# Kernel optimization log

Hardware: AMD Instinct MI355X
Metric: run time of the kernel (lower is better)

Reference implementation:

```python
import jax, jax.numpy as jnp
import numpy as np

N_NODES = 2048
N_EDGES = 32768
N_IN = 256
MSG_HID = 512
MSG_OUT = 256
N_HID = 512


def _linear_params(key, fan_in, fan_out):
    kw, kb = jax.random.split(key)
    bound = 1.0 / np.sqrt(fan_in)
    W = jax.random.uniform(kw, (fan_out, fan_in), jnp.float32, -bound, bound)
    b = jax.random.uniform(kb, (fan_out,), jnp.float32, -bound, bound)
    return W, b


def setup_inputs() -> dict:
    key = jax.random.key(0)
    ks = jax.random.split(key, 8)
    inputs = jax.random.normal(ks[0], (N_NODES, N_IN), jnp.float32)
    # one-hot incidence matrices built from random receiver/sender node indices
    recv_idx = jax.random.randint(ks[1], (N_EDGES,), 0, N_NODES)
    send_idx = jax.random.randint(ks[2], (N_EDGES,), 0, N_NODES)
    rel_rec = jax.nn.one_hot(recv_idx, N_NODES, dtype=jnp.float32)   # [E, N]
    rel_send = jax.nn.one_hot(send_idx, N_NODES, dtype=jnp.float32)  # [E, N]
    msg_W1, msg_b1 = _linear_params(ks[3], 2 * N_IN, MSG_HID)
    msg_W2, msg_b2 = _linear_params(ks[4], MSG_HID, MSG_OUT)
    out_W1, out_b1 = _linear_params(ks[5], N_IN + MSG_OUT, N_HID)
    out_W2, out_b2 = _linear_params(ks[6], N_HID, N_HID)
    out_W3, out_b3 = _linear_params(ks[7], N_HID, N_IN)
    return {
        'inputs': inputs, 'rel_rec': rel_rec, 'rel_send': rel_send,
        'msg_W1': msg_W1, 'msg_b1': msg_b1, 'msg_W2': msg_W2, 'msg_b2': msg_b2,
        'out_W1': out_W1, 'out_b1': out_b1, 'out_W2': out_W2, 'out_b2': out_b2,
        'out_W3': out_W3, 'out_b3': out_b3,
    }


def reference(inputs, rel_rec, rel_send, msg_W1, msg_b1, msg_W2, msg_b2,
              out_W1, out_b1, out_W2, out_b2, out_W3, out_b3):
    # gather node features to edges via dense one-hot matmuls (as in original)
    receivers = rel_rec @ inputs    # [E, n_in]
    senders = rel_send @ inputs     # [E, n_in]
    pre_msg = jnp.concatenate([senders, receivers], axis=1)  # [E, 2*n_in]
    # edge-message MLP (dropout p=0 -> identity)
    msg = jax.nn.relu(pre_msg @ msg_W1.T + msg_b1)
    msg = jax.nn.relu(msg @ msg_W2.T + msg_b2)               # [E, msg_out]
    # scatter-add messages to receiving nodes: (msg^T @ rel_rec)^T == rel_rec^T @ msg
    agg_msgs = rel_rec.T @ msg                               # [N, msg_out]
    aug_inputs = jnp.concatenate([inputs, agg_msgs], axis=-1)
    # node-update MLP
    pred = jax.nn.relu(aug_inputs @ out_W1.T + out_b1)
    pred = jax.nn.relu(pred @ out_W2.T + out_b2)
    pred = pred @ out_W3.T + out_b3
    return inputs + pred
```

## Files before the change

### kernel.cpp

```cpp
#include <hip/hip_runtime.h>
#include <hip/hip_bf16.h>
#include <stdint.h>

using bf16 = __hip_bfloat16;
typedef short bf16x8 __attribute__((ext_vector_type(8)));
typedef float floatx4 __attribute__((ext_vector_type(4)));

static constexpr int NODES = 2048;
static constexpr int EDGES = 32768;

__device__ inline uint4 cvt8(const float* __restrict__ p) {
    const float4* f = (const float4*)p;
    float4 a = f[0], b = f[1];
    union { uint4 u; bf16 h[8]; } pk;
    pk.h[0] = __float2bfloat16(a.x); pk.h[1] = __float2bfloat16(a.y);
    pk.h[2] = __float2bfloat16(a.z); pk.h[3] = __float2bfloat16(a.w);
    pk.h[4] = __float2bfloat16(b.x); pk.h[5] = __float2bfloat16(b.y);
    pk.h[6] = __float2bfloat16(b.z); pk.h[7] = __float2bfloat16(b.w);
    return pk.u;
}

template<int BM, int BN, int AMODE, int BMODE, int EPI>
__device__ __forceinline__ void gemm_body(
    const bf16* __restrict__ A, const float* __restrict__ Af,
    const float* __restrict__ Bt, const float* __restrict__ bias,
    bf16* __restrict__ Cout, float* __restrict__ OutF,
    const float* __restrict__ inputsF, const float* __restrict__ UV,
    const float* __restrict__ b1v, const int* __restrict__ sidx,
    const int* __restrict__ ridx, const float* __restrict__ aggin,
    float* __restrict__ aggout, int M, int N, int K, int bx, int by)
{
    constexpr int BK = 32;
    constexpr int PA = BM / 64;
    constexpr int PB = BN / 64;
    constexpr int MI = BM / 32;
    constexpr int NJ = BN / 32;
    __shared__ bf16 As[BM * BK];
    __shared__ bf16 Bs[BN * BK];
    __shared__ int sIdx[BM];
    __shared__ int rIdx[BM];

    const int t = threadIdx.x;
    const int m0 = by * BM;
    const int n0 = bx * BN;

    if constexpr (AMODE == 3) {
        if (t < BM) {
            sIdx[t] = sidx[m0 + t] & (NODES - 1);
            rIdx[t] = ridx[m0 + t] & (NODES - 1);
        }
        __syncthreads();
    }

    const int sr = t >> 2;
    const int sc = t & 3;

    uint4 ra[PA], rb[PB];

    auto loadTiles = [&](int kt) {
        const int kk = kt * BK + sc * 8;
#pragma unroll
        for (int p = 0; p < PA; ++p) {
            const int row = p * 64 + sr;
            if constexpr (AMODE == 0) {
                ra[p] = *(const uint4*)(A + (size_t)(m0 + row) * K + kk);
            } else if constexpr (AMODE == 1) {
                ra[p] = cvt8(Af + (size_t)(m0 + row) * K + kk);
            } else if constexpr (AMODE == 2) {
                const float* src = (kk < 256)
                    ? (inputsF + (size_t)(m0 + row) * 256 + kk)
                    : (aggin + (size_t)(m0 + row) * 256 + (kk - 256));
                ra[p] = cvt8(src);
            } else {
                const float4* u = (const float4*)(UV + (size_t)sIdx[row] * 1024 + kk);
                const float4* v = (const float4*)(UV + (size_t)rIdx[row] * 1024 + 512 + kk);
                const float4* c = (const float4*)(b1v + kk);
                float4 u0 = u[0], u1 = u[1], v0 = v[0], v1 = v[1], c0 = c[0], c1 = c[1];
                union { uint4 q; bf16 h[8]; } pk;
                pk.h[0] = __float2bfloat16(fmaxf(u0.x + v0.x + c0.x, 0.f));
                pk.h[1] = __float2bfloat16(fmaxf(u0.y + v0.y + c0.y, 0.f));
                pk.h[2] = __float2bfloat16(fmaxf(u0.z + v0.z + c0.z, 0.f));
                pk.h[3] = __float2bfloat16(fmaxf(u0.w + v0.w + c0.w, 0.f));
                pk.h[4] = __float2bfloat16(fmaxf(u1.x + v1.x + c1.x, 0.f));
                pk.h[5] = __float2bfloat16(fmaxf(u1.y + v1.y + c1.y, 0.f));
                pk.h[6] = __float2bfloat16(fmaxf(u1.z + v1.z + c1.z, 0.f));
                pk.h[7] = __float2bfloat16(fmaxf(u1.w + v1.w + c1.w, 0.f));
                ra[p] = pk.q;
            }
        }
#pragma unroll
        for (int p = 0; p < PB; ++p) {
            const int row = p * 64 + sr;
            if constexpr (BMODE == 0) {
                rb[p] = cvt8(Bt + (size_t)(n0 + row) * K + kk);
            } else {
                const int n = n0 + row;
                rb[p] = cvt8(Bt + (size_t)(n & 511) * 512 + (n >> 9) * 256 + kk);
            }
        }
    };

    const int wv = t >> 6;
    const int lane = t & 63;
    const int wm = wv >> 1, wn = wv & 1;
    const int r16 = lane & 15, q = lane >> 4;

    floatx4 acc[MI][NJ] = {};

    loadTiles(0);
    const int KT = K / BK;
    for (int kt = 0; kt < KT; ++kt) {
        __syncthreads();
#pragma unroll
        for (int p = 0; p < PA; ++p)
            *(uint4*)(&As[(p * 64 + sr) * BK + sc * 8]) = ra[p];
#pragma unroll
        for (int p = 0; p < PB; ++p)
            *(uint4*)(&Bs[(p * 64 + sr) * BK + sc * 8]) = rb[p];
        __syncthreads();
        if (kt + 1 < KT) loadTiles(kt + 1);

        bf16x8 af[MI], bfr[NJ];
#pragma unroll
        for (int i = 0; i < MI; ++i)
            af[i] = *(const bf16x8*)(&As[(wm * (BM / 2) + i * 16 + r16) * BK + q * 8]);
#pragma unroll
        for (int j = 0; j < NJ; ++j)
            bfr[j] = *(const bf16x8*)(&Bs[(wn * (BN / 2) + j * 16 + r16) * BK + q * 8]);
#pragma unroll
        for (int i = 0; i < MI; ++i)
#pragma unroll
            for (int j = 0; j < NJ; ++j)
                acc[i][j] = __builtin_amdgcn_mfma_f32_16x16x32_bf16(af[i], bfr[j], acc[i][j], 0, 0, 0);
    }

    float bv[NJ];
#pragma unroll
    for (int j = 0; j < NJ; ++j)
        bv[j] = (EPI == 3) ? 0.f : bias[n0 + wn * (BN / 2) + j * 16 + r16];

#pragma unroll
    for (int i = 0; i < MI; ++i) {
        const int lr = wm * (BM / 2) + i * 16 + q * 4;
        const int rbase = m0 + lr;
#pragma unroll
        for (int j = 0; j < NJ; ++j) {
            const int gc = n0 + wn * (BN / 2) + j * 16 + r16;
#pragma unroll
            for (int r = 0; r < 4; ++r) {
                float v = acc[i][j][r] + bv[j];
                const int gr = rbase + r;
                if constexpr (EPI == 0) {
                    v = fmaxf(v, 0.0f);
                    Cout[(size_t)gr * N + gc] = __float2bfloat16(v);
                } else if constexpr (EPI == 1) {
                    v = fmaxf(v, 0.0f);
                    atomicAdd(&aggout[(size_t)rIdx[lr + r] * 256 + gc], v);
                } else if constexpr (EPI == 2) {
                    OutF[(size_t)gr * 256 + gc] = inputsF[(size_t)gr * 256 + gc] + v;
                } else {
                    OutF[(size_t)gr * N + gc] = v;
                }
            }
        }
    }
}

template<int BM, int BN, int AMODE, int BMODE, int EPI>
__global__ __launch_bounds__(256, 2) void gemm_k(
    const bf16* __restrict__ A, const float* __restrict__ Af,
    const float* __restrict__ Bt, const float* __restrict__ bias,
    bf16* __restrict__ Cout, float* __restrict__ OutF,
    const float* __restrict__ inputsF, const float* __restrict__ UV,
    const float* __restrict__ b1v, const int* __restrict__ sidx,
    const int* __restrict__ ridx, const float* __restrict__ aggin,
    float* __restrict__ aggout, int M, int N, int K)
{
    gemm_body<BM, BN, AMODE, BMODE, EPI>(A, Af, Bt, bias, Cout, OutF, inputsF,
        UV, b1v, sidx, ridx, aggin, aggout, M, N, K, blockIdx.x, blockIdx.y);
}

__global__ __launch_bounds__(256) void fat_pre(
    const float* __restrict__ rel_rec, const float* __restrict__ rel_send,
    int* __restrict__ recv_idx, int* __restrict__ send_idx,
    float4* __restrict__ agg, const float* __restrict__ inputs,
    const float* __restrict__ msg_W1, float* __restrict__ UV)
{
    const int b = blockIdx.x;
    if (b < 16384) {
        const int half = b >> 13;
        const int rb = b & 8191;
        const float* mat = half ? rel_send : rel_rec;
        int* out = half ? send_idx : recv_idx;
        const int w = threadIdx.x >> 6;
        const int lane = threadIdx.x & 63;
        const int row = rb * 4 + w;
        if (lane == 0) out[row] = 0;
        const uint4* base = (const uint4*)(mat + (size_t)row * NODES);
        for (int p = 0; p < 8; ++p) {
            uint4 v = base[p * 64 + lane];
            const bool hit = (v.x | v.y | v.z | v.w) != 0u;
            if (hit) {
                int e = v.x ? 0 : (v.y ? 1 : (v.z ? 2 : 3));
                out[row] = p * 256 + lane * 4 + e;
            }
            if (__any(hit)) break;
        }
    } else if (b < 16896) {
        agg[(size_t)(b - 16384) * 256 + threadIdx.x] = float4{0.f, 0.f, 0.f, 0.f};
    } else {
        const int g = b - 16896;
        gemm_body<64, 64, 1, 1, 3>(nullptr, inputs, msg_W1, nullptr, nullptr, UV,
            nullptr, nullptr, nullptr, nullptr, nullptr, nullptr, nullptr,
            NODES, 1024, 256, g & 15, g >> 4);
    }
}

extern "C" void kernel_launch(void* const* d_in, const int* in_sizes, int n_in,
                              void* d_out, int out_size, void* d_ws, size_t ws_size,
                              hipStream_t stream) {
    const float* inputs   = (const float*)d_in[0];
    const float* rel_rec  = (const float*)d_in[1];
    const float* rel_send = (const float*)d_in[2];
    const float* msg_W1   = (const float*)d_in[3];
    const float* msg_b1   = (const float*)d_in[4];
    const float* msg_W2   = (const float*)d_in[5];
    const float* msg_b2   = (const float*)d_in[6];
    const float* out_W1   = (const float*)d_in[7];
    const float* out_b1   = (const float*)d_in[8];
    const float* out_W2   = (const float*)d_in[9];
    const float* out_b2   = (const float*)d_in[10];
    const float* out_W3   = (const float*)d_in[11];
    const float* out_b3   = (const float*)d_in[12];

    char* ws = (char*)d_ws;
    int*   recv_idx = (int*)(ws + 0);
    int*   send_idx = (int*)(ws + 131072);
    float* agg      = (float*)(ws + 262144);
    float* UV       = (float*)(ws + 2359296);
    bf16*  g1       = (bf16*)(ws + 10747904);
    bf16*  g2       = (bf16*)(ws + 12845056);
    if (ws_size < (size_t)16 * 1024 * 1024) return;

    fat_pre<<<17408, 256, 0, stream>>>(rel_rec, rel_send, recv_idx, send_idx,
                                       (float4*)agg, inputs, msg_W1, UV);

    gemm_k<128, 128, 3, 0, 1><<<dim3(2, 256), 256, 0, stream>>>(
        nullptr, nullptr, msg_W2, msg_b2, nullptr, nullptr,
        nullptr, UV, msg_b1, send_idx, recv_idx, nullptr, agg,
        EDGES, 256, 512);

    gemm_k<64, 64, 2, 0, 0><<<dim3(8, 32), 256, 0, stream>>>(
        nullptr, nullptr, out_W1, out_b1, g1, nullptr,
        inputs, nullptr, nullptr, nullptr, nullptr, agg, nullptr,
        NODES, 512, 512);

    gemm_k<64, 64, 0, 0, 0><<<dim3(8, 32), 256, 0, stream>>>(
        g1, nullptr, out_W2, out_b2, g2, nullptr,
        nullptr, nullptr, nullptr, nullptr, nullptr, nullptr, nullptr,
        NODES, 512, 512);

    gemm_k<64, 64, 0, 0, 2><<<dim3(4, 32), 256, 0, stream>>>(
        g2, nullptr, out_W3, out_b3, nullptr, (float*)d_out,
        inputs, nullptr, nullptr, nullptr, nullptr, nullptr, nullptr,
        NODES, 256, 512);
}
```

Before: 602.6 us.

## Store per-node UV projections in bf16 and retile edge GEMM to 64x256

The per-node first-layer projections (UV) are now written in bf16 instead of fp32, which halves the bytes of the random-row gathers the edge-message GEMM does per edge. The gathered values are widened back to fp32 by bit-shifting before the bias add and ReLU. The edge GEMM also changes from 128x128 tiles on a 2x256 grid to 64x256 tiles on a 1x512 grid, so each gathered row is loaded once across all 256 output columns instead of twice. The cost is extra rounding of UV to bf16 before the add, which costs some accuracy, and a larger accumulator tile per wave.

```diff
diff --git a/kernel.cpp b/kernel.cpp
--- a/kernel.cpp
+++ b/kernel.cpp
@@ -25,7 +25,7 @@
     const bf16* __restrict__ A, const float* __restrict__ Af,
     const float* __restrict__ Bt, const float* __restrict__ bias,
     bf16* __restrict__ Cout, float* __restrict__ OutF,
-    const float* __restrict__ inputsF, const float* __restrict__ UV,
+    const float* __restrict__ inputsF, const bf16* __restrict__ UVb,
     const float* __restrict__ b1v, const int* __restrict__ sidx,
     const int* __restrict__ ridx, const float* __restrict__ aggin,
     float* __restrict__ aggout, int M, int N, int K, int bx, int by)
@@ -72,19 +72,20 @@
                     : (aggin + (size_t)(m0 + row) * 256 + (kk - 256));
                 ra[p] = cvt8(src);
             } else {
-                const float4* u = (const float4*)(UV + (size_t)sIdx[row] * 1024 + kk);
-                const float4* v = (const float4*)(UV + (size_t)rIdx[row] * 1024 + 512 + kk);
+                union { uint4 q; unsigned short h[8]; } uu, vv;
+                uu.q = *(const uint4*)(UVb + (size_t)sIdx[row] * 1024 + kk);
+                vv.q = *(const uint4*)(UVb + (size_t)rIdx[row] * 1024 + 512 + kk);
                 const float4* c = (const float4*)(b1v + kk);
-                float4 u0 = u[0], u1 = u[1], v0 = v[0], v1 = v[1], c0 = c[0], c1 = c[1];
+                float4 c0 = c[0], c1 = c[1];
+                const float cf[8] = {c0.x, c0.y, c0.z, c0.w, c1.x, c1.y, c1.z, c1.w};
                 union { uint4 q; bf16 h[8]; } pk;
-                pk.h[0] = __float2bfloat16(fmaxf(u0.x + v0.x + c0.x, 0.f));
-                pk.h[1] = __float2bfloat16(fmaxf(u0.y + v0.y + c0.y, 0.f));
-                pk.h[2] = __float2bfloat16(fmaxf(u0.z + v0.z + c0.z, 0.f));
-                pk.h[3] = __float2bfloat16(fmaxf(u0.w + v0.w + c0.w, 0.f));
-                pk.h[4] = __float2bfloat16(fmaxf(u1.x + v1.x + c1.x, 0.f));
-                pk.h[5] = __float2bfloat16(fmaxf(u1.y + v1.y + c1.y, 0.f));
-                pk.h[6] = __float2bfloat16(fmaxf(u1.z + v1.z + c1.z, 0.f));
-                pk.h[7] = __float2bfloat16(fmaxf(u1.w + v1.w + c1.w, 0.f));
+#pragma unroll
+                for (int e = 0; e < 8; ++e) {
+                    union { unsigned int u; float f; } a2, b2;
+                    a2.u = (unsigned int)uu.h[e] << 16;
+                    b2.u = (unsigned int)vv.h[e] << 16;
+                    pk.h[e] = __float2bfloat16(fmaxf(a2.f + b2.f + cf[e], 0.f));
+                }
                 ra[p] = pk.q;
             }
         }
@@ -137,7 +138,7 @@
     float bv[NJ];
 #pragma unroll
     for (int j = 0; j < NJ; ++j)
-        bv[j] = (EPI == 3) ? 0.f : bias[n0 + wn * (BN / 2) + j * 16 + r16];
+        bv[j] = (EPI == 3 || EPI == 4) ? 0.f : bias[n0 + wn * (BN / 2) + j * 16 + r16];
 
 #pragma unroll
     for (int i = 0; i < MI; ++i) {
@@ -158,8 +159,10 @@
                     atomicAdd(&aggout[(size_t)rIdx[lr + r] * 256 + gc], v);
                 } else if constexpr (EPI == 2) {
                     OutF[(size_t)gr * 256 + gc] = inputsF[(size_t)gr * 256 + gc] + v;
+                } else if constexpr (EPI == 3) {
+                    OutF[(size_t)gr * N + gc] = v;
                 } else {
-                    OutF[(size_t)gr * N + gc] = v;
+                    Cout[(size_t)gr * N + gc] = __float2bfloat16(v);
                 }
             }
         }
@@ -171,20 +174,20 @@
     const bf16* __restrict__ A, const float* __restrict__ Af,
     const float* __restrict__ Bt, const float* __restrict__ bias,
     bf16* __restrict__ Cout, float* __restrict__ OutF,
-    const float* __restrict__ inputsF, const float* __restrict__ UV,
+    const float* __restrict__ inputsF, const bf16* __restrict__ UVb,
     const float* __restrict__ b1v, const int* __restrict__ sidx,
     const int* __restrict__ ridx, const float* __restrict__ aggin,
     float* __restrict__ aggout, int M, int N, int K)
 {
     gemm_body<BM, BN, AMODE, BMODE, EPI>(A, Af, Bt, bias, Cout, OutF, inputsF,
-        UV, b1v, sidx, ridx, aggin, aggout, M, N, K, blockIdx.x, blockIdx.y);
+        UVb, b1v, sidx, ridx, aggin, aggout, M, N, K, blockIdx.x, blockIdx.y);
 }
 
 __global__ __launch_bounds__(256) void fat_pre(
     const float* __restrict__ rel_rec, const float* __restrict__ rel_send,
     int* __restrict__ recv_idx, int* __restrict__ send_idx,
     float4* __restrict__ agg, const float* __restrict__ inputs,
-    const float* __restrict__ msg_W1, float* __restrict__ UV)
+    const float* __restrict__ msg_W1, bf16* __restrict__ UVb)
 {
     const int b = blockIdx.x;
     if (b < 16384) {
@@ -210,7 +213,7 @@
         agg[(size_t)(b - 16384) * 256 + threadIdx.x] = float4{0.f, 0.f, 0.f, 0.f};
     } else {
         const int g = b - 16896;
-        gemm_body<64, 64, 1, 1, 3>(nullptr, inputs, msg_W1, nullptr, nullptr, UV,
+        gemm_body<64, 64, 1, 1, 4>(nullptr, inputs, msg_W1, nullptr, UVb, nullptr,
             nullptr, nullptr, nullptr, nullptr, nullptr, nullptr, nullptr,
             NODES, 1024, 256, g & 15, g >> 4);
     }
@@ -237,17 +240,17 @@
     int*   recv_idx = (int*)(ws + 0);
     int*   send_idx = (int*)(ws + 131072);
     float* agg      = (float*)(ws + 262144);
-    float* UV       = (float*)(ws + 2359296);
-    bf16*  g1       = (bf16*)(ws + 10747904);
-    bf16*  g2       = (bf16*)(ws + 12845056);
-    if (ws_size < (size_t)16 * 1024 * 1024) return;
+    bf16*  UVb      = (bf16*)(ws + 2359296);
+    bf16*  g1       = (bf16*)(ws + 6553600);
+    bf16*  g2       = (bf16*)(ws + 8650752);
+    if (ws_size < (size_t)11 * 1024 * 1024) return;
 
     fat_pre<<<17408, 256, 0, stream>>>(rel_rec, rel_send, recv_idx, send_idx,
-                                       (float4*)agg, inputs, msg_W1, UV);
-
-    gemm_k<128, 128, 3, 0, 1><<<dim3(2, 256), 256, 0, stream>>>(
+                                       (float4*)agg, inputs, msg_W1, UVb);
+
+    gemm_k<64, 256, 3, 0, 1><<<dim3(1, 512), 256, 0, stream>>>(
         nullptr, nullptr, msg_W2, msg_b2, nullptr, nullptr,
-        nullptr, UV, msg_b1, send_idx, recv_idx, nullptr, agg,
+        nullptr, UVb, msg_b1, send_idx, recv_idx, nullptr, agg,
         EDGES, 256, 512);
 
     gemm_k<64, 64, 2, 0, 0><<<dim3(8, 32), 256, 0, stream>>>(
```

Measured after the change: 609.2 us. About the same (+1.1%).
